# Kernel tuning notes

Measured on AMD Instinct MI355X. Metric: run time of the kernel, lower is better.

The kernel has to match this reference:

```python
import jax, jax.numpy as jnp
import numpy as np

B, S, H = 1, 2048, 4096
NQ, NKV, HD = 32, 8, 128
BLOCK = 128            # block size of block_streaming_attn_func
SINK_BLOCKS = 1        # sink_size 128 / BLOCK
LOCAL_BLOCKS = 8       # local_window_size 1024 / BLOCK
ROPE_BASE = 10000.0


def setup_inputs() -> dict:
    key = jax.random.key(0)
    ks = jax.random.split(key, 5)
    s = 0.02
    return {
        "hidden_states": jax.random.normal(ks[0], (B, S, H), jnp.float32),
        "wq": jax.random.normal(ks[1], (H, NQ * HD), jnp.float32) * s,
        "wk": jax.random.normal(ks[2], (H, NKV * HD), jnp.float32) * s,
        "wv": jax.random.normal(ks[3], (H, NKV * HD), jnp.float32) * s,
        "wo": jax.random.normal(ks[4], (NQ * HD, H), jnp.float32) * s,
    }


def _rope(x):
    # x: [B, S, heads, HD]; non-interleaved (GPT-NeoX half-split) rotary, full head_dim
    pos = jnp.arange(S, dtype=jnp.float32)
    inv = 1.0 / (ROPE_BASE ** (jnp.arange(0, HD, 2, dtype=jnp.float32) / HD))
    f = pos[:, None] * inv[None, :]                 # [S, HD/2]
    cos = jnp.cos(f)[None, :, None, :]
    sin = jnp.sin(f)[None, :, None, :]
    x1, x2 = x[..., : HD // 2], x[..., HD // 2 :]
    return jnp.concatenate([x1 * cos - x2 * sin, x2 * cos + x1 * sin], axis=-1).astype(x.dtype)


def _streaming_mask():
    # causal + (sink blocks OR local window blocks), block granularity = BLOCK
    idx = jnp.arange(S)
    blk = idx // BLOCK
    causal = idx[None, :] <= idx[:, None]
    sink = blk[None, :] < SINK_BLOCKS
    local = (blk[:, None] - blk[None, :]) < LOCAL_BLOCKS
    return causal & (sink | local)                  # [S, S]


def reference(hidden_states, wq, wk, wv, wo):
    q = (hidden_states @ wq).reshape(B, S, NQ, HD)
    k = (hidden_states @ wk).reshape(B, S, NKV, HD)
    v = (hidden_states @ wv).reshape(B, S, NKV, HD)
    q = _rope(q)
    k = _rope(k)
    rep = NQ // NKV                                 # repeat_kv (GQA)
    k = jnp.repeat(k, rep, axis=2)
    v = jnp.repeat(v, rep, axis=2)
    scores = jnp.einsum('bqhd,bkhd->bhqk', q, k) / jnp.sqrt(jnp.float32(HD))
    mask = _streaming_mask()
    scores = jnp.where(mask[None, None], scores, jnp.finfo(scores.dtype).min)
    p = jax.nn.softmax(scores, axis=-1)
    out = jnp.einsum('bhqk,bkhd->bqhd', p, v).reshape(B, S, NQ * HD)
    return out @ wo
```

## Files before the change

### kernel.cpp

```cpp
#include <hip/hip_runtime.h>
#include <hip/hip_bf16.h>
#include <math.h>

typedef __bf16 bf16;
typedef __attribute__((ext_vector_type(8))) __bf16 bf16x8;
typedef __attribute__((ext_vector_type(4))) __bf16 bf16x4;
typedef __attribute__((ext_vector_type(4))) float f32x4;

#define MFMA16(a, b, c) __builtin_amdgcn_mfma_f32_16x16x32_bf16(a, b, c, 0, 0, 0)

__device__ __forceinline__ void load16_lds(const bf16* g, bf16* l) {
  __builtin_amdgcn_global_load_lds(
      (const __attribute__((address_space(1))) void*)g,
      (__attribute__((address_space(3))) void*)l, 16, 0, 0);
}

__global__ __launch_bounds__(256) void cast_k(const float* __restrict__ src,
                                              bf16* __restrict__ dst) {
  const size_t i = ((size_t)blockIdx.x * 256 + threadIdx.x) * 8;
  f32x4 a = *(const f32x4*)(src + i);
  f32x4 b = *(const f32x4*)(src + i + 4);
  bf16x8 h;
#pragma unroll
  for (int j = 0; j < 4; ++j) {
    h[j] = (bf16)a[j];
    h[4 + j] = (bf16)b[j];
  }
  *(bf16x8*)(dst + i) = h;
}

__global__ __launch_bounds__(256) void transpose_cast_k(
    const float* __restrict__ src, bf16* __restrict__ dst, int rows,
    int cols) {
  __shared__ float tile[64][65];
  const int c0 = blockIdx.x * 64, r0 = blockIdx.y * 64;
  const int tid = threadIdx.x;
  const int lr = tid >> 4;
  const int lc = (tid & 15) * 4;
#pragma unroll
  for (int i = 0; i < 4; ++i) {
    const int row = lr + i * 16;
    const f32x4 v = *(const f32x4*)&src[(size_t)(r0 + row) * cols + c0 + lc];
#pragma unroll
    for (int j = 0; j < 4; ++j) tile[row][lc + j] = v[j];
  }
  __syncthreads();
#pragma unroll
  for (int i = 0; i < 4; ++i) {
    const int orow = lr + i * 16;
    bf16x4 h;
#pragma unroll
    for (int j = 0; j < 4; ++j) h[j] = (bf16)tile[lc + j][orow];
    *(bf16x4*)&dst[(size_t)(c0 + orow) * rows + r0 + lc] = h;
  }
}

#define BARX() __builtin_amdgcn_s_barrier()
#define SBAR0() __builtin_amdgcn_sched_barrier(0)
#define LGKM0()                                       \
  {                                                   \
    asm volatile("s_waitcnt lgkmcnt(0)" ::: "memory");\
    SBAR0();                                          \
  }
#define VMC(N)                                          \
  {                                                     \
    asm volatile("s_waitcnt vmcnt(" #N ")" ::: "memory");\
    SBAR0();                                            \
  }

#define DS_A(BUF, QM)                                                       \
  {                                                                         \
    _Pragma("unroll") for (int mi = 0; mi < 4; ++mi)                        \
        _Pragma("unroll") for (int kk = 0; kk < 2; ++kk)                    \
            a[mi][kk] = *(const bf16x8*)&As[BUF][(aBase ^ (kk << 5)) +      \
                                                (QM)*4096 + mi * 1024];     \
  }

#define DS_B(BUF, QN, BR)                                                   \
  {                                                                         \
    _Pragma("unroll") for (int ni = 0; ni < 2; ++ni)                        \
        _Pragma("unroll") for (int kk = 0; kk < 2; ++kk)                    \
            BR[ni][kk] = *(const bf16x8*)&Bs[BUF][(bBase ^ (kk << 5)) +     \
                                                  (QN)*2048 + ni * 1024];   \
  }

#define MMAC(QM, QN, BR)                                                    \
  {                                                                         \
    __builtin_amdgcn_s_setprio(1);                                          \
    _Pragma("unroll") for (int mi = 0; mi < 4; ++mi)                        \
        _Pragma("unroll") for (int ni = 0; ni < 2; ++ni) {                  \
      acc[(QM)*4 + mi][(QN)*2 + ni] =                                       \
          MFMA16(a[mi][0], BR[ni][0], acc[(QM)*4 + mi][(QN)*2 + ni]);       \
      acc[(QM)*4 + mi][(QN)*2 + ni] =                                       \
          MFMA16(a[mi][1], BR[ni][1], acc[(QM)*4 + mi][(QN)*2 + ni]);       \
    }                                                                       \
    __builtin_amdgcn_s_setprio(0);                                          \
  }

#define STAGE_A(BUF, T)                                                     \
  {                                                                         \
    const bf16* g0 = aS0 + (size_t)(T)*64;                                  \
    const bf16* g1 = aS1 + (size_t)(T)*64;                                  \
    bf16* l = &As[BUF][w * 512];                                            \
    load16_lds(g0, l);                                                      \
    load16_lds(g1, l + 4096);                                               \
    load16_lds(g0 + ROWK128, l + 8192);                                     \
    load16_lds(g1 + ROWK128, l + 12288);                                    \
  }

#define STAGE_B(BUF, T)                                                     \
  {                                                                         \
    const bf16* g0 = bS0 + (size_t)(T)*64;                                  \
    const bf16* g1 = bS1 + (size_t)(T)*64;                                  \
    bf16* l = &Bs[BUF][w * 512];                                            \
    load16_lds(g0, l);                                                      \
    load16_lds(g1, l + 4096);                                               \
    load16_lds(g0 + ROWK128, l + 8192);                                     \
    load16_lds(g1 + ROWK128, l + 12288);                                    \
  }

__global__ __launch_bounds__(512, 2) void gemm_qkv256(
    const bf16* __restrict__ A, const bf16* __restrict__ Bt,
    bf16* __restrict__ Cq, bf16* __restrict__ Ck, bf16* __restrict__ Cv) {
  constexpr int K = 4096;
  constexpr size_t ROWK128 = (size_t)128 * K;
  __shared__ bf16 As[2][256 * 64];
  __shared__ bf16 Bs[2][256 * 64];

  const int tid = threadIdx.x;
  const int lane = tid & 63;
  const int w = tid >> 6;
  const int wm = w >> 2;
  const int wn = w & 3;
  const int quad = lane >> 4;
  const int m16 = lane & 15;

  const int rowBase = blockIdx.y * 256;
  const int colBase = blockIdx.x * 256;

  const int u0 = tid, u1 = 512 + tid;
  const int r0 = u0 >> 3, c0s = (u0 & 7) ^ (r0 & 7);
  const int r1 = u1 >> 3, c1s = (u1 & 7) ^ (r1 & 7);
  const bf16* aS0 = A + (size_t)(rowBase + r0) * K + c0s * 8;
  const bf16* aS1 = A + (size_t)(rowBase + r1) * K + c1s * 8;
  const bf16* bS0 = Bt + (size_t)(colBase + r0) * K + c0s * 8;
  const bf16* bS1 = Bt + (size_t)(colBase + r1) * K + c1s * 8;

  const int xsw = (m16 & 7) << 3;
  const int ko0 = (quad * 8) ^ xsw;
  const int aBase = (wm * 128 + m16) * 64 + ko0;
  const int bBase = (wn * 64 + m16) * 64 + ko0;

  f32x4 acc[8][4];
#pragma unroll
  for (int i = 0; i < 8; ++i)
#pragma unroll
    for (int j = 0; j < 4; ++j) acc[i][j] = (f32x4){0.f, 0.f, 0.f, 0.f};

  bf16x8 a[4][2], b0[2][2], b1[2][2];

  STAGE_A(0, 0);
  STAGE_B(0, 0);
  STAGE_A(1, 1);
  STAGE_B(1, 1);
  VMC(8);
  BARX();

  constexpr int nT = K / 64;
#pragma unroll 1
  for (int i = 0; i < nT / 2; ++i) {
    const int p0 = (2 * i + 2 < nT) ? 2 * i + 2 : 0;
    const int p1 = (2 * i + 3 < nT) ? 2 * i + 3 : 0;
    DS_A(0, 0);
    DS_B(0, 0, b0);
    BARX();
    LGKM0();
    MMAC(0, 0, b0);
    BARX();
    DS_B(0, 1, b1);
    BARX();
    LGKM0();
    MMAC(0, 1, b1);
    BARX();
    DS_A(0, 1);
    STAGE_B(0, p0);
    BARX();
    LGKM0();
    MMAC(1, 0, b0);
    BARX();
    STAGE_A(0, p0);
    VMC(6);
    BARX();
    MMAC(1, 1, b1);
    BARX();
    DS_A(1, 0);
    DS_B(1, 0, b0);
    BARX();
    LGKM0();
    MMAC(0, 0, b0);
    BARX();
    DS_B(1, 1, b1);
    BARX();
    LGKM0();
    MMAC(0, 1, b1);
    BARX();
    DS_A(1, 1);
    STAGE_B(1, p1);
    BARX();
    LGKM0();
    MMAC(1, 0, b0);
    BARX();
    STAGE_A(1, p1);
    VMC(6);
    BARX();
    MMAC(1, 1, b1);
    BARX();
  }
  VMC(0);

#pragma unroll
  for (int am = 0; am < 8; ++am) {
    const int gr0 = rowBase + wm * 128 + am * 16 + quad * 4;
#pragma unroll
    for (int an = 0; an < 4; ++an) {
      const int gc = colBase + wn * 64 + an * 16 + m16;
      if (colBase < 4096) {
#pragma unroll
        for (int r = 0; r < 4; ++r)
          Cq[(size_t)(gr0 + r) * 4096 + gc] = (bf16)acc[am][an][r];
      } else if (colBase < 5120) {
#pragma unroll
        for (int r = 0; r < 4; ++r)
          Ck[(size_t)(gr0 + r) * 1024 + (gc - 4096)] = (bf16)acc[am][an][r];
      } else {
        bf16x4 h;
#pragma unroll
        for (int r = 0; r < 4; ++r) h[r] = (bf16)acc[am][an][r];
        *(bf16x4*)&Cv[(size_t)(gc - 5120) * 2048 + gr0] = h;
      }
    }
  }
}

template <typename OT, int EPI>
__global__ __launch_bounds__(256, 2) void gemm_bt(const bf16* __restrict__ A,
                                                  const bf16* __restrict__ Bt,
                                                  OT* __restrict__ C,
                                                  bf16* __restrict__ Ck,
                                                  bf16* __restrict__ C2, int M,
                                                  int N, int K, int ldc) {
  __shared__ bf16 As[128 * 32];
  __shared__ bf16 Bs[128 * 32];

  const int tid = threadIdx.x;
  const int lane = tid & 63;
  const int w = tid >> 6;
  const int quad = lane >> 4;
  const int m16 = lane & 15;
  const int wr = (w >> 1) * 64;
  const int wc = (w & 1) * 64;
  const int rowBase = blockIdx.y * 128;
  const int colBase = blockIdx.x * 128;

  f32x4 acc[4][4];
#pragma unroll
  for (int i = 0; i < 4; ++i)
#pragma unroll
    for (int j = 0; j < 4; ++j) acc[i][j] = (f32x4){0.f, 0.f, 0.f, 0.f};

  const int u1 = w * 128 + lane;
  const int u2 = u1 + 64;
  const int r1 = u1 >> 2, s1 = (u1 & 3) * 8;
  const int r2 = u2 >> 2, s2 = (u2 & 3) * 8;
  const bf16* aG1 = A + (size_t)(rowBase + r1) * K + s1;
  const bf16* aG2 = A + (size_t)(rowBase + r2) * K + s2;
  const bf16* bG1 = Bt + (size_t)(colBase + r1) * K + s1;
  const bf16* bG2 = Bt + (size_t)(colBase + r2) * K + s2;
  bf16* const lA1 = As + (size_t)(w * 128) * 8;
  bf16* const lA2 = As + (size_t)(w * 128 + 64) * 8;
  bf16* const lB1 = Bs + (size_t)(w * 128) * 8;
  bf16* const lB2 = Bs + (size_t)(w * 128 + 64) * 8;

  for (int k0 = 0; k0 < K; k0 += 32) {
    load16_lds(aG1 + k0, lA1);
    load16_lds(aG2 + k0, lA2);
    load16_lds(bG1 + k0, lB1);
    load16_lds(bG2 + k0, lB2);
    __syncthreads();

    bf16x8 af[4], bfr[4];
#pragma unroll
    for (int mi = 0; mi < 4; ++mi)
      af[mi] = *(const bf16x8*)&As[(wr + mi * 16 + m16) * 32 + quad * 8];
#pragma unroll
    for (int ni = 0; ni < 4; ++ni)
      bfr[ni] = *(const bf16x8*)&Bs[(wc + ni * 16 + m16) * 32 + quad * 8];
#pragma unroll
    for (int mi = 0; mi < 4; ++mi)
#pragma unroll
      for (int ni = 0; ni < 4; ++ni)
        acc[mi][ni] = MFMA16(af[mi], bfr[ni], acc[mi][ni]);
    __syncthreads();
  }

#pragma unroll
  for (int mi = 0; mi < 4; ++mi) {
#pragma unroll
    for (int ni = 0; ni < 4; ++ni) {
      const int gr0 = rowBase + wr + mi * 16 + quad * 4;
      const int gc = colBase + wc + ni * 16 + m16;
      if constexpr (EPI == 0) {
#pragma unroll
        for (int r = 0; r < 4; ++r)
          C[(size_t)(gr0 + r) * ldc + gc] = (OT)acc[mi][ni][r];
      }
    }
  }
}

__global__ __launch_bounds__(256) void rope_k(bf16* __restrict__ qb,
                                              bf16* __restrict__ kb) {
  const int NQTOT = 2048 * 32 * 64;
  const int NKTOT = 2048 * 8 * 64;
  int idx = blockIdx.x * 256 + threadIdx.x;
  bf16* buf;
  int nh, rest;
  if (idx < NQTOT) {
    buf = qb;
    nh = 32;
    rest = idx;
  } else {
    rest = idx - NQTOT;
    if (rest >= NKTOT) return;
    buf = kb;
    nh = 8;
  }
  const int j = rest & 63;
  const int hs = rest >> 6;
  const int hh = hs % nh;
  const int s = hs / nh;
  const float inv = __expf((float)j * -0.14391157f);
  const float f = (float)s * inv;
  float sn, cs;
  __sincosf(f, &sn, &cs);
  const size_t base = (size_t)(s * nh + hh) * 128 + j;
  const float x1 = (float)buf[base];
  const float x2 = (float)buf[base + 64];
  buf[base] = (bf16)(x1 * cs - x2 * sn);
  buf[base + 64] = (bf16)(x2 * cs + x1 * sn);
}

__global__ __launch_bounds__(256, 2) void attn_k(const bf16* __restrict__ q,
                                                 const bf16* __restrict__ kbuf,
                                                 const bf16* __restrict__ vT,
                                                 bf16* __restrict__ attn) {
  const int qb = 15 - blockIdx.x;
  const int h = blockIdx.y;
  const int kvh = h >> 2;
  const int tid = threadIdx.x;
  const int lane = tid & 63;
  const int w = tid >> 6;
  const int quad = lane >> 4;
  const int m16 = lane & 15;

  __shared__ bf16 Ks[4][64 * 32];
  __shared__ bf16 Vs[2][128 * 32];
  __shared__ bf16 Ps[128][72];

  const int qrow0 = qb * 128 + w * 32;

  bf16x8 qf[2][4];
#pragma unroll
  for (int rt = 0; rt < 2; ++rt)
#pragma unroll
    for (int kt = 0; kt < 4; ++kt)
      qf[rt][kt] = *(const bf16x8*)&q[(size_t)(qrow0 + rt * 16 + m16) * 4096 +
                                      h * 128 + kt * 32 + quad * 8];

  f32x4 o[2][8];
  float lsum[2][4];
#pragma unroll
  for (int rt = 0; rt < 2; ++rt) {
#pragma unroll
    for (int dt = 0; dt < 8; ++dt) o[rt][dt] = (f32x4){0.f, 0.f, 0.f, 0.f};
#pragma unroll
    for (int r = 0; r < 4; ++r) lsum[rt][r] = 0.f;
  }

  const float scale = 0.08838834764831845f;
  const bf16* kbase = kbuf + kvh * 128;
  const bf16* vbase = vT + (size_t)(kvh * 128) * 2048;

  const int klocal = (lane >> 2);
  const int kseg = (lane & 3) * 8;

  for (int b = 0; b <= qb; ++b) {
    if (b > 0 && (qb - b) >= 8) continue;
    const bool diag = (b == qb);
    for (int half = 0; half < 2; ++half) {
      const int gk0 = b * 128 + half * 64;

#pragma unroll
      for (int i = 0; i < 4; ++i) {
        const int j = w * 4 + i;
        const int kt = j >> 2, grp = (j & 3) * 16;
        load16_lds(kbase + (size_t)(gk0 + grp + klocal) * 1024 + kt * 32 + kseg,
                   &Ks[kt][grp * 32]);
      }
#pragma unroll
      for (int i = 0; i < 4; ++i) {
        const int j = w * 4 + i;
        const int kc = j >> 3, grp = (j & 7) * 16;
        load16_lds(vbase + (size_t)(grp + klocal) * 2048 + gk0 + kc * 32 + kseg,
                   &Vs[kc][grp * 32]);
      }
      __syncthreads();

      const bool skip = diag && (half * 64 > w * 32 + 31);
      if (!skip) {
        f32x4 sc[2][4];
#pragma unroll
        for (int rt = 0; rt < 2; ++rt)
#pragma unroll
          for (int ct = 0; ct < 4; ++ct)
            sc[rt][ct] = (f32x4){0.f, 0.f, 0.f, 0.f};
#pragma unroll
        for (int kt = 0; kt < 4; ++kt) {
          bf16x8 kf[4];
#pragma unroll
          for (int ct = 0; ct < 4; ++ct)
            kf[ct] = *(const bf16x8*)&Ks[kt][(ct * 16 + m16) * 32 + quad * 8];
#pragma unroll
          for (int rt = 0; rt < 2; ++rt)
#pragma unroll
            for (int ct = 0; ct < 4; ++ct)
              sc[rt][ct] = MFMA16(qf[rt][kt], kf[ct], sc[rt][ct]);
        }

#pragma unroll
        for (int rt = 0; rt < 2; ++rt)
#pragma unroll
          for (int ct = 0; ct < 4; ++ct)
#pragma unroll
            for (int r = 0; r < 4; ++r) {
              float p = __expf(sc[rt][ct][r] * scale);
              if (diag) {
                const int colg = gk0 + ct * 16 + m16;
                const int rowg = qrow0 + rt * 16 + quad * 4 + r;
                if (colg > rowg) p = 0.f;
              }
              lsum[rt][r] += p;
              Ps[w * 32 + rt * 16 + quad * 4 + r][ct * 16 + m16] = (bf16)p;
            }

#pragma unroll
        for (int rt = 0; rt < 2; ++rt)
#pragma unroll
          for (int kc = 0; kc < 2; ++kc) {
            const bf16x8 pa =
                *(const bf16x8*)&Ps[w * 32 + rt * 16 + m16][kc * 32 + quad * 8];
#pragma unroll
            for (int dt = 0; dt < 8; ++dt) {
              const bf16x8 vb =
                  *(const bf16x8*)&Vs[kc][(dt * 16 + m16) * 32 + quad * 8];
              o[rt][dt] = MFMA16(pa, vb, o[rt][dt]);
            }
          }
      }
      __syncthreads();
    }
  }

#pragma unroll
  for (int rt = 0; rt < 2; ++rt) {
    float inv[4];
#pragma unroll
    for (int r = 0; r < 4; ++r) {
      float s = lsum[rt][r];
      s += __shfl_xor(s, 1);
      s += __shfl_xor(s, 2);
      s += __shfl_xor(s, 4);
      s += __shfl_xor(s, 8);
      inv[r] = 1.0f / s;
    }
#pragma unroll
    for (int dt = 0; dt < 8; ++dt)
#pragma unroll
      for (int r = 0; r < 4; ++r)
        attn[(size_t)(qrow0 + rt * 16 + quad * 4 + r) * 4096 + h * 128 +
             dt * 16 + m16] = (bf16)(o[rt][dt][r] * inv[r]);
  }
}

extern "C" void kernel_launch(void* const* d_in, const int* in_sizes, int n_in,
                              void* d_out, int out_size, void* d_ws,
                              size_t ws_size, hipStream_t stream) {
  const float* hidden = (const float*)d_in[0];
  const float* wq = (const float*)d_in[1];
  const float* wk = (const float*)d_in[2];
  const float* wv = (const float*)d_in[3];
  const float* wo = (const float*)d_in[4];
  float* out = (float*)d_out;

  const size_t MB = 1024 * 1024;
  bf16* hiddenB = (bf16*)d_ws;
  bf16* wqkvT = (bf16*)((char*)d_ws + 16 * MB);
  bf16* woT = (bf16*)d_ws;
  bf16* attnb = (bf16*)((char*)d_ws + 32 * MB);
  bf16* qbuf = (bf16*)((char*)d_ws + 64 * MB);
  bf16* kbuf = (bf16*)((char*)d_ws + 80 * MB);
  bf16* vT = (bf16*)((char*)d_ws + 84 * MB);

  cast_k<<<4096, 256, 0, stream>>>(hidden, hiddenB);
  transpose_cast_k<<<dim3(64, 64), 256, 0, stream>>>(wq, wqkvT, 4096, 4096);
  transpose_cast_k<<<dim3(16, 64), 256, 0, stream>>>(
      wk, wqkvT + (size_t)4096 * 4096, 4096, 1024);
  transpose_cast_k<<<dim3(16, 64), 256, 0, stream>>>(
      wv, wqkvT + (size_t)5120 * 4096, 4096, 1024);

  gemm_qkv256<<<dim3(24, 8), 512, 0, stream>>>(hiddenB, wqkvT, qbuf, kbuf, vT);

  rope_k<<<(2048 * 32 * 64 + 2048 * 8 * 64) / 256, 256, 0, stream>>>(qbuf,
                                                                     kbuf);

  transpose_cast_k<<<dim3(64, 64), 256, 0, stream>>>(wo, woT, 4096, 4096);

  attn_k<<<dim3(16, 32), 256, 0, stream>>>(qbuf, kbuf, vT, attnb);

  gemm_bt<float, 0><<<dim3(32, 16), 256, 0, stream>>>(
      attnb, woT, out, nullptr, nullptr, 2048, 4096, 4096, 4096);
}
```

Baseline: 476.1 us.

## Generalize 256-row pipelined GEMM to variable N-tile and use for QKV and output projections

Turns the hand-pipelined 256x256 QKV GEMM into a template with a configurable N-tile (192 or 128 columns). The QKV projection now runs on 256 workgroups of 256x192 tiles, up from 192, to fill more compute units. The simple 128x128 output-projection GEMM is replaced by the same pipelined kernel with 256x128 tiles, which brings the LDS-direct double buffering and swizzled layout to that GEMM. The vmcnt waits change with the number of in-flight loads, and the sched_barrier fences are removed, which gives the compiler more freedom but may change instruction ordering.

```diff
diff --git a/kernel.cpp b/kernel.cpp
--- a/kernel.cpp
+++ b/kernel.cpp
@@ -56,17 +56,10 @@
 }
 
 #define BARX() __builtin_amdgcn_s_barrier()
-#define SBAR0() __builtin_amdgcn_sched_barrier(0)
-#define LGKM0()                                       \
-  {                                                   \
-    asm volatile("s_waitcnt lgkmcnt(0)" ::: "memory");\
-    SBAR0();                                          \
-  }
-#define VMC(N)                                          \
-  {                                                     \
-    asm volatile("s_waitcnt vmcnt(" #N ")" ::: "memory");\
-    SBAR0();                                            \
-  }
+#define LGKM0() asm volatile("s_waitcnt lgkmcnt(0)" ::: "memory")
+#define VMC7() asm volatile("s_waitcnt vmcnt(7)" ::: "memory")
+#define VMC6() asm volatile("s_waitcnt vmcnt(6)" ::: "memory")
+#define VMC0() asm volatile("s_waitcnt vmcnt(0)" ::: "memory")
 
 #define DS_A(BUF, QM)                                                       \
   {                                                                         \
@@ -76,23 +69,23 @@
                                                 (QM)*4096 + mi * 1024];     \
   }
 
-#define DS_B(BUF, QN, BR)                                                   \
+#define DS_B(BUF, NOFF, BR, NH)                                             \
   {                                                                         \
-    _Pragma("unroll") for (int ni = 0; ni < 2; ++ni)                        \
+    _Pragma("unroll") for (int ni = 0; ni < (NH); ++ni)                     \
         _Pragma("unroll") for (int kk = 0; kk < 2; ++kk)                    \
             BR[ni][kk] = *(const bf16x8*)&Bs[BUF][(bBase ^ (kk << 5)) +     \
-                                                  (QN)*2048 + ni * 1024];   \
-  }
-
-#define MMAC(QM, QN, BR)                                                    \
+                                                  ((NOFF) + ni) * 1024];    \
+  }
+
+#define MMAC(QM, NOFF, BR, NH)                                              \
   {                                                                         \
     __builtin_amdgcn_s_setprio(1);                                          \
     _Pragma("unroll") for (int mi = 0; mi < 4; ++mi)                        \
-        _Pragma("unroll") for (int ni = 0; ni < 2; ++ni) {                  \
-      acc[(QM)*4 + mi][(QN)*2 + ni] =                                       \
-          MFMA16(a[mi][0], BR[ni][0], acc[(QM)*4 + mi][(QN)*2 + ni]);       \
-      acc[(QM)*4 + mi][(QN)*2 + ni] =                                       \
-          MFMA16(a[mi][1], BR[ni][1], acc[(QM)*4 + mi][(QN)*2 + ni]);       \
+        _Pragma("unroll") for (int ni = 0; ni < (NH); ++ni) {               \
+      acc[(QM)*4 + mi][(NOFF) + ni] =                                       \
+          MFMA16(a[mi][0], BR[ni][0], acc[(QM)*4 + mi][(NOFF) + ni]);       \
+      acc[(QM)*4 + mi][(NOFF) + ni] =                                       \
+          MFMA16(a[mi][1], BR[ni][1], acc[(QM)*4 + mi][(NOFF) + ni]);       \
     }                                                                       \
     __builtin_amdgcn_s_setprio(0);                                          \
   }
@@ -110,22 +103,22 @@
 
 #define STAGE_B(BUF, T)                                                     \
   {                                                                         \
-    const bf16* g0 = bS0 + (size_t)(T)*64;                                  \
-    const bf16* g1 = bS1 + (size_t)(T)*64;                                  \
-    bf16* l = &Bs[BUF][w * 512];                                            \
-    load16_lds(g0, l);                                                      \
-    load16_lds(g1, l + 4096);                                               \
-    load16_lds(g0 + ROWK128, l + 8192);                                     \
-    load16_lds(g1 + ROWK128, l + 12288);                                    \
-  }
-
-__global__ __launch_bounds__(512, 2) void gemm_qkv256(
+    _Pragma("unroll") for (int j = 0; j < NFRAG; ++j)                       \
+        load16_lds(bS0 + (size_t)(T)*64 + (size_t)j * 64 * K,               \
+                   &Bs[BUF][j * 4096 + w * 512]);                           \
+  }
+
+template <typename OT, int NFRAG, int EPI>
+__global__ __launch_bounds__(512, 2) void gemm256(
     const bf16* __restrict__ A, const bf16* __restrict__ Bt,
-    bf16* __restrict__ Cq, bf16* __restrict__ Ck, bf16* __restrict__ Cv) {
-  constexpr int K = 4096;
-  constexpr size_t ROWK128 = (size_t)128 * K;
+    OT* __restrict__ C, bf16* __restrict__ Ck, bf16* __restrict__ Cv, int K,
+    int ldc) {
+  constexpr int BN = NFRAG * 64;
+  constexpr int BH0 = (NFRAG + 1) / 2;
+  constexpr int BH1 = NFRAG - BH0;
+  const size_t ROWK128 = (size_t)128 * K;
   __shared__ bf16 As[2][256 * 64];
-  __shared__ bf16 Bs[2][256 * 64];
+  __shared__ bf16 Bs[2][BN * 64];
 
   const int tid = threadIdx.x;
   const int lane = tid & 63;
@@ -136,7 +129,7 @@
   const int m16 = lane & 15;
 
   const int rowBase = blockIdx.y * 256;
-  const int colBase = blockIdx.x * 256;
+  const int colBase = blockIdx.x * BN;
 
   const int u0 = tid, u1 = 512 + tid;
   const int r0 = u0 >> 3, c0s = (u0 & 7) ^ (r0 & 7);
@@ -144,175 +137,105 @@
   const bf16* aS0 = A + (size_t)(rowBase + r0) * K + c0s * 8;
   const bf16* aS1 = A + (size_t)(rowBase + r1) * K + c1s * 8;
   const bf16* bS0 = Bt + (size_t)(colBase + r0) * K + c0s * 8;
-  const bf16* bS1 = Bt + (size_t)(colBase + r1) * K + c1s * 8;
 
   const int xsw = (m16 & 7) << 3;
   const int ko0 = (quad * 8) ^ xsw;
   const int aBase = (wm * 128 + m16) * 64 + ko0;
-  const int bBase = (wn * 64 + m16) * 64 + ko0;
-
-  f32x4 acc[8][4];
+  const int bBase = (wn * (16 * NFRAG) + m16) * 64 + ko0;
+
+  f32x4 acc[8][NFRAG];
 #pragma unroll
   for (int i = 0; i < 8; ++i)
 #pragma unroll
-    for (int j = 0; j < 4; ++j) acc[i][j] = (f32x4){0.f, 0.f, 0.f, 0.f};
-
-  bf16x8 a[4][2], b0[2][2], b1[2][2];
+    for (int j = 0; j < NFRAG; ++j) acc[i][j] = (f32x4){0.f, 0.f, 0.f, 0.f};
+
+  bf16x8 a[4][2], b0[BH0][2], b1[BH1 > 0 ? BH1 : 1][2];
 
   STAGE_A(0, 0);
   STAGE_B(0, 0);
   STAGE_A(1, 1);
   STAGE_B(1, 1);
-  VMC(8);
+  if constexpr (NFRAG == 3) VMC7(); else VMC6();
   BARX();
 
-  constexpr int nT = K / 64;
+  const int nT = K / 64;
 #pragma unroll 1
   for (int i = 0; i < nT / 2; ++i) {
     const int p0 = (2 * i + 2 < nT) ? 2 * i + 2 : 0;
     const int p1 = (2 * i + 3 < nT) ? 2 * i + 3 : 0;
     DS_A(0, 0);
-    DS_B(0, 0, b0);
-    BARX();
-    LGKM0();
-    MMAC(0, 0, b0);
-    BARX();
-    DS_B(0, 1, b1);
-    BARX();
-    LGKM0();
-    MMAC(0, 1, b1);
+    DS_B(0, 0, b0, BH0);
+    BARX();
+    LGKM0();
+    MMAC(0, 0, b0, BH0);
+    BARX();
+    DS_B(0, BH0, b1, BH1);
+    BARX();
+    LGKM0();
+    MMAC(0, BH0, b1, BH1);
     BARX();
     DS_A(0, 1);
     STAGE_B(0, p0);
     BARX();
     LGKM0();
-    MMAC(1, 0, b0);
+    MMAC(1, 0, b0, BH0);
     BARX();
     STAGE_A(0, p0);
-    VMC(6);
-    BARX();
-    MMAC(1, 1, b1);
+    if constexpr (NFRAG == 3) VMC7(); else VMC6();
+    BARX();
+    MMAC(1, BH0, b1, BH1);
     BARX();
     DS_A(1, 0);
-    DS_B(1, 0, b0);
-    BARX();
-    LGKM0();
-    MMAC(0, 0, b0);
-    BARX();
-    DS_B(1, 1, b1);
-    BARX();
-    LGKM0();
-    MMAC(0, 1, b1);
+    DS_B(1, 0, b0, BH0);
+    BARX();
+    LGKM0();
+    MMAC(0, 0, b0, BH0);
+    BARX();
+    DS_B(1, BH0, b1, BH1);
+    BARX();
+    LGKM0();
+    MMAC(0, BH0, b1, BH1);
     BARX();
     DS_A(1, 1);
     STAGE_B(1, p1);
     BARX();
     LGKM0();
-    MMAC(1, 0, b0);
+    MMAC(1, 0, b0, BH0);
     BARX();
     STAGE_A(1, p1);
-    VMC(6);
-    BARX();
-    MMAC(1, 1, b1);
-    BARX();
-  }
-  VMC(0);
+    if constexpr (NFRAG == 3) VMC7(); else VMC6();
+    BARX();
+    MMAC(1, BH0, b1, BH1);
+    BARX();
+  }
+  VMC0();
 
 #pragma unroll
   for (int am = 0; am < 8; ++am) {
     const int gr0 = rowBase + wm * 128 + am * 16 + quad * 4;
 #pragma unroll
-    for (int an = 0; an < 4; ++an) {
-      const int gc = colBase + wn * 64 + an * 16 + m16;
-      if (colBase < 4096) {
+    for (int an = 0; an < NFRAG; ++an) {
+      const int base16 = colBase + wn * (16 * NFRAG) + an * 16;
+      const int gc = base16 + m16;
+      if constexpr (EPI == 0) {
 #pragma unroll
         for (int r = 0; r < 4; ++r)
-          Cq[(size_t)(gr0 + r) * 4096 + gc] = (bf16)acc[am][an][r];
-      } else if (colBase < 5120) {
-#pragma unroll
-        for (int r = 0; r < 4; ++r)
-          Ck[(size_t)(gr0 + r) * 1024 + (gc - 4096)] = (bf16)acc[am][an][r];
+          C[(size_t)(gr0 + r) * ldc + gc] = (OT)acc[am][an][r];
       } else {
-        bf16x4 h;
-#pragma unroll
-        for (int r = 0; r < 4; ++r) h[r] = (bf16)acc[am][an][r];
-        *(bf16x4*)&Cv[(size_t)(gc - 5120) * 2048 + gr0] = h;
-      }
-    }
-  }
-}
-
-template <typename OT, int EPI>
-__global__ __launch_bounds__(256, 2) void gemm_bt(const bf16* __restrict__ A,
-                                                  const bf16* __restrict__ Bt,
-                                                  OT* __restrict__ C,
-                                                  bf16* __restrict__ Ck,
-                                                  bf16* __restrict__ C2, int M,
-                                                  int N, int K, int ldc) {
-  __shared__ bf16 As[128 * 32];
-  __shared__ bf16 Bs[128 * 32];
-
-  const int tid = threadIdx.x;
-  const int lane = tid & 63;
-  const int w = tid >> 6;
-  const int quad = lane >> 4;
-  const int m16 = lane & 15;
-  const int wr = (w >> 1) * 64;
-  const int wc = (w & 1) * 64;
-  const int rowBase = blockIdx.y * 128;
-  const int colBase = blockIdx.x * 128;
-
-  f32x4 acc[4][4];
-#pragma unroll
-  for (int i = 0; i < 4; ++i)
-#pragma unroll
-    for (int j = 0; j < 4; ++j) acc[i][j] = (f32x4){0.f, 0.f, 0.f, 0.f};
-
-  const int u1 = w * 128 + lane;
-  const int u2 = u1 + 64;
-  const int r1 = u1 >> 2, s1 = (u1 & 3) * 8;
-  const int r2 = u2 >> 2, s2 = (u2 & 3) * 8;
-  const bf16* aG1 = A + (size_t)(rowBase + r1) * K + s1;
-  const bf16* aG2 = A + (size_t)(rowBase + r2) * K + s2;
-  const bf16* bG1 = Bt + (size_t)(colBase + r1) * K + s1;
-  const bf16* bG2 = Bt + (size_t)(colBase + r2) * K + s2;
-  bf16* const lA1 = As + (size_t)(w * 128) * 8;
-  bf16* const lA2 = As + (size_t)(w * 128 + 64) * 8;
-  bf16* const lB1 = Bs + (size_t)(w * 128) * 8;
-  bf16* const lB2 = Bs + (size_t)(w * 128 + 64) * 8;
-
-  for (int k0 = 0; k0 < K; k0 += 32) {
-    load16_lds(aG1 + k0, lA1);
-    load16_lds(aG2 + k0, lA2);
-    load16_lds(bG1 + k0, lB1);
-    load16_lds(bG2 + k0, lB2);
-    __syncthreads();
-
-    bf16x8 af[4], bfr[4];
-#pragma unroll
-    for (int mi = 0; mi < 4; ++mi)
-      af[mi] = *(const bf16x8*)&As[(wr + mi * 16 + m16) * 32 + quad * 8];
-#pragma unroll
-    for (int ni = 0; ni < 4; ++ni)
-      bfr[ni] = *(const bf16x8*)&Bs[(wc + ni * 16 + m16) * 32 + quad * 8];
-#pragma unroll
-    for (int mi = 0; mi < 4; ++mi)
-#pragma unroll
-      for (int ni = 0; ni < 4; ++ni)
-        acc[mi][ni] = MFMA16(af[mi], bfr[ni], acc[mi][ni]);
-    __syncthreads();
-  }
-
-#pragma unroll
-  for (int mi = 0; mi < 4; ++mi) {
-#pragma unroll
-    for (int ni = 0; ni < 4; ++ni) {
-      const int gr0 = rowBase + wr + mi * 16 + quad * 4;
-      const int gc = colBase + wc + ni * 16 + m16;
-      if constexpr (EPI == 0) {
-#pragma unroll
-        for (int r = 0; r < 4; ++r)
-          C[(size_t)(gr0 + r) * ldc + gc] = (OT)acc[mi][ni][r];
+        if (base16 < 4096) {
+#pragma unroll
+          for (int r = 0; r < 4; ++r)
+            C[(size_t)(gr0 + r) * 4096 + gc] = (OT)acc[am][an][r];
+        } else if (base16 < 5120) {
+#pragma unroll
+          for (int r = 0; r < 4; ++r)
+            Ck[(size_t)(gr0 + r) * 1024 + (gc - 4096)] = (bf16)acc[am][an][r];
+        } else {
+          bf16x4 h;
+#pragma unroll
+          for (int r = 0; r < 4; ++r) h[r] = (bf16)acc[am][an][r];
+          *(bf16x4*)&Cv[(size_t)(gc - 5120) * 2048 + gr0] = h;
+        }
       }
     }
   }
@@ -518,7 +441,8 @@
   transpose_cast_k<<<dim3(16, 64), 256, 0, stream>>>(
       wv, wqkvT + (size_t)5120 * 4096, 4096, 1024);
 
-  gemm_qkv256<<<dim3(24, 8), 512, 0, stream>>>(hiddenB, wqkvT, qbuf, kbuf, vT);
+  gemm256<bf16, 3, 2><<<dim3(32, 8), 512, 0, stream>>>(hiddenB, wqkvT, qbuf,
+                                                       kbuf, vT, 4096, 4096);
 
   rope_k<<<(2048 * 32 * 64 + 2048 * 8 * 64) / 256, 256, 0, stream>>>(qbuf,
                                                                      kbuf);
@@ -527,6 +451,6 @@
 
   attn_k<<<dim3(16, 32), 256, 0, stream>>>(qbuf, kbuf, vT, attnb);
 
-  gemm_bt<float, 0><<<dim3(32, 16), 256, 0, stream>>>(
-      attnb, woT, out, nullptr, nullptr, 2048, 4096, 4096, 4096);
-}
+  gemm256<float, 2, 0><<<dim3(32, 8), 512, 0, stream>>>(
+      attnb, woT, out, nullptr, nullptr, 4096, 4096);
+}
```

Result: faster. 448.9 us (-5.7%).
